# Optimization experiments

Hardware: AMD Instinct MI355X
Metric: run time of the kernel (lower is better)

## Reference

```python
import jax, jax.numpy as jnp
import numpy as np

INF = 1e+24
DK = 16


def setup_inputs() -> dict:
    key = jax.random.key(0)
    ks = jax.random.split(key, 9)
    B, T, D = 64, 512, 1024
    x = jax.random.normal(ks[0], (B, T, D), dtype=jnp.float32)
    padding_mask = jax.random.randint(ks[1], (B, T, 1), 0, 2) > 0
    s = 1.0 / np.sqrt(D)
    Wq = jax.random.normal(ks[2], (D, DK), dtype=jnp.float32) * s
    bq = jnp.zeros((DK,), dtype=jnp.float32)
    Wk = jax.random.normal(ks[3], (D, DK), dtype=jnp.float32) * s
    bk = jnp.zeros((DK,), dtype=jnp.float32)
    Wv = jax.random.normal(ks[4], (D, D), dtype=jnp.float32) * s
    bv = jnp.zeros((D,), dtype=jnp.float32)
    return {"x": x, "padding_mask": padding_mask, "Wq": Wq, "bq": bq,
            "Wk": Wk, "bk": bk, "Wv": Wv, "bv": bv}


def reference(x, padding_mask, Wq, bq, Wk, bk, Wv, bv):
    # x: [B,T,D]; padding_mask: [B,T,1] bool
    q = x @ Wq + bq                      # [B,T,dk]
    k = x @ Wk + bk                      # [B,T,dk]
    v = x @ Wv + bv                      # [B,T,D]
    # original writes -INF into k at padded positions (broadcast over dk)
    k = jnp.where(padding_mask, jnp.float32(-INF), k)
    # NOTE: original multiplies by sqrt(dk) (misnamed _inv_dk)
    att = jnp.einsum('btd,bsd->bts', q, k) * jnp.sqrt(jnp.float32(DK))
    T = x.shape[1]
    causal = jnp.triu(jnp.ones((T, T), dtype=bool), k=1)  # [T,T]
    att = jnp.where(causal[None, :, :], jnp.float32(-INF), att)
    return jnp.einsum('bts,bsd->btd', jax.nn.softmax(att, axis=2), v)
```

## Files before the change

kernel.cpp:

```cpp
#include <hip/hip_runtime.h>
#include <hip/hip_bf16.h>
#include <stdint.h>

#define NEG_BIG (-1e24f)

typedef __attribute__((ext_vector_type(8))) short bf16x8;
typedef __attribute__((ext_vector_type(4))) float f32x4;

#define AS1 __attribute__((address_space(1)))
#define AS3 __attribute__((address_space(3)))

__device__ __forceinline__ void gload_lds16(const void* g, void* l) {
    __builtin_amdgcn_global_load_lds((AS1 unsigned*)g, (AS3 unsigned*)l, 16, 0, 0);
}

__device__ __forceinline__ unsigned short f2bf(float f) {
    union { float f; unsigned u; } v; v.f = f;
    return (unsigned short)((v.u + 0x7FFFu + ((v.u >> 16) & 1u)) >> 16);
}

__device__ __forceinline__ void lds_barrier() {
    asm volatile("s_waitcnt lgkmcnt(0)" ::: "memory");
    __builtin_amdgcn_s_barrier();
    asm volatile("" ::: "memory");
}

__global__ void detect_mask_kernel(const unsigned* pm, int* flag) {
    __shared__ int notI, notF;
    if (threadIdx.x == 0) { notI = 0; notF = 0; }
    __syncthreads();
    int li = 0, lf = 0;
    for (int i = threadIdx.x; i < 8192; i += 256) {
        unsigned v = pm[i];
        if (v > 1u) li = 1;
        if (v != 0u && v != 0x3F800000u) lf = 1;
    }
    if (li) atomicOr(&notI, 1);
    if (lf) atomicOr(&notF, 1);
    __syncthreads();
    if (threadIdx.x == 0) *flag = notI ? (notF ? 1 : 2) : 0;
}

__global__ __launch_bounds__(1024, 8)
void qk_conv_kernel(const float* __restrict__ x,
                    const float* __restrict__ Wq, const float* __restrict__ bq,
                    const float* __restrict__ Wk, const float* __restrict__ bk,
                    const void* __restrict__ pm, const int* __restrict__ pmflag,
                    unsigned short* __restrict__ xbf,
                    float* __restrict__ qo, float* __restrict__ ko) {
    __shared__ float smem[4 * 64 * 33];
    const int tid = threadIdx.x;
    const int r0 = blockIdx.x * 64;
    const int lane = tid & 63;
    const int wv = __builtin_amdgcn_readfirstlane(tid >> 6);
    const int g = wv & 3;
    const int sl = wv >> 2;
    const int jb = (g & 1) * 8;
    const int d0 = sl * 16;
    const float* __restrict__ W = (g < 2) ? Wq : Wk;

    const int sr = tid >> 4;
    const int sd = (tid & 15) * 4;
    const float* __restrict__ xp = x + (size_t)(r0 + sr) * 1024 + sd;
    unsigned short* __restrict__ xbp = xbf + (size_t)(r0 + sr) * 1024 + sd;

    float acc[8];
#pragma unroll
    for (int j = 0; j < 8; j++) acc[j] = 0.f;

    float4 xv = *(const float4*)xp;
    {
        uint2 pk;
        pk.x = (unsigned)f2bf(xv.x) | ((unsigned)f2bf(xv.y) << 16);
        pk.y = (unsigned)f2bf(xv.z) | ((unsigned)f2bf(xv.w) << 16);
        *(uint2*)xbp = pk;
        float* b0 = smem;
        b0[sr * 65 + sd + 0] = xv.x;
        b0[sr * 65 + sd + 1] = xv.y;
        b0[sr * 65 + sd + 2] = xv.z;
        b0[sr * 65 + sd + 3] = xv.w;
    }
    xv = *(const float4*)(xp + 64);
    lds_barrier();

    for (int t = 0; t < 16; t++) {
        if (t + 1 < 16) {
            uint2 pk;
            pk.x = (unsigned)f2bf(xv.x) | ((unsigned)f2bf(xv.y) << 16);
            pk.y = (unsigned)f2bf(xv.z) | ((unsigned)f2bf(xv.w) << 16);
            *(uint2*)(xbp + (t + 1) * 64) = pk;
            float* bw = smem + ((t + 1) & 1) * (64 * 65);
            bw[sr * 65 + sd + 0] = xv.x;
            bw[sr * 65 + sd + 1] = xv.y;
            bw[sr * 65 + sd + 2] = xv.z;
            bw[sr * 65 + sd + 3] = xv.w;
            if (t + 2 < 16) xv = *(const float4*)(xp + (t + 2) * 64);
        }
        const float* __restrict__ xrow = smem + (t & 1) * (64 * 65) + lane * 65 + d0;
        const float* __restrict__ wrow = W + (size_t)(t * 64 + d0) * 16 + jb;
#pragma unroll
        for (int dd = 0; dd < 16; dd += 2) {
            const float x0 = xrow[dd];
            const float x1 = xrow[dd + 1];
            const float* __restrict__ w0 = wrow + dd * 16;
#pragma unroll
            for (int j = 0; j < 8; j++) acc[j] = fmaf(x0, w0[j], acc[j]);
#pragma unroll
            for (int j = 0; j < 8; j++) acc[j] = fmaf(x1, w0[16 + j], acc[j]);
        }
        lds_barrier();
    }

    float* red = smem;
    const int cb = jb + (g >> 1) * 16;
    {
        float* rr = red + ((size_t)(sl * 64 + lane)) * 33 + cb;
#pragma unroll
        for (int j = 0; j < 8; j++) rr[j] = acc[j];
    }
    __syncthreads();

    const int row = tid >> 4;
    const int c = tid & 15;
    const int grow = r0 + row;
    const float qv = red[(size_t)row * 33 + c]
                   + red[(size_t)(64 + row) * 33 + c]
                   + red[(size_t)(128 + row) * 33 + c]
                   + red[(size_t)(192 + row) * 33 + c] + bq[c];
    qo[(size_t)grow * 16 + c] = qv;
    const int flag = *pmflag;
    bool mk;
    if (flag == 1) mk = ((const unsigned char*)pm)[grow] != 0;
    else           mk = ((const unsigned*)pm)[grow] != 0;
    float kv;
    if (mk) {
        kv = NEG_BIG;
    } else {
        kv = red[(size_t)row * 33 + 16 + c]
           + red[(size_t)(64 + row) * 33 + 16 + c]
           + red[(size_t)(128 + row) * 33 + 16 + c]
           + red[(size_t)(192 + row) * 33 + 16 + c] + bk[c];
    }
    ko[(size_t)grow * 16 + c] = kv;
}

__global__ void wvt_kernel(const float* __restrict__ Wv, unsigned short* __restrict__ WvT) {
    __shared__ float tile[32][33];
    const int k0 = blockIdx.x * 32, n0 = blockIdx.y * 32;
    const int tid = threadIdx.x;
#pragma unroll
    for (int i = 0; i < 4; i++) {
        int idx = i * 256 + tid;
        int r = idx >> 5, c = idx & 31;
        tile[r][c] = Wv[(size_t)(k0 + r) * 1024 + n0 + c];
    }
    __syncthreads();
#pragma unroll
    for (int i = 0; i < 4; i++) {
        int idx = i * 256 + tid;
        int r = idx >> 5, c = idx & 31;
        WvT[(size_t)(n0 + r) * 1024 + k0 + c] = f2bf(tile[c][r]);
    }
}

__global__ __launch_bounds__(256, 4)
void vgemm_kernel(const unsigned short* __restrict__ A,
                  const unsigned short* __restrict__ Bt,
                  const float* __restrict__ bias,
                  unsigned short* __restrict__ vTg) {
    __shared__ __align__(16) unsigned short smem[17408];
    const int bid = blockIdx.x;
    const int c = bid & 7;
    const int g = bid >> 3;
    const int mt = c * 32 + (g >> 3);
    const int nt = g & 7;
    const int m0 = mt * 128;
    const int n0 = nt * 128;
    const int tid = threadIdx.x;
    const int lane = tid & 63;
    const int wave = tid >> 6;
    const int wm = (wave & 1) * 64;
    const int wn = (wave >> 1) * 64;
    const int l15 = lane & 15;
    const int quad = lane >> 4;
    const int arow = tid >> 2;
    const int acol = (tid & 3) * 8;
    const unsigned short* __restrict__ Ar0 = A + (size_t)(m0 + arow) * 1024 + acol;
    const unsigned short* __restrict__ Ar1 = A + (size_t)(m0 + 64 + arow) * 1024 + acol;
    const unsigned short* __restrict__ Br0 = Bt + (size_t)(n0 + arow) * 1024 + acol;
    const unsigned short* __restrict__ Br1 = Bt + (size_t)(n0 + 64 + arow) * 1024 + acol;
    f32x4 acc[4][4];
#pragma unroll
    for (int i = 0; i < 4; i++)
#pragma unroll
        for (int j = 0; j < 4; j++)
#pragma unroll
            for (int r = 0; r < 4; r++) acc[i][j][r] = 0.f;

    {
        unsigned short* As = smem;
        unsigned short* Bs = smem + 4096;
        gload_lds16(Ar0, As + tid * 8);
        gload_lds16(Ar1, As + 2048 + tid * 8);
        gload_lds16(Br0, Bs + tid * 8);
        gload_lds16(Br1, Bs + 2048 + tid * 8);
    }
    __syncthreads();
    int cur = 0;
    for (int t = 0; t < 32; t++) {
        if (t + 1 < 32) {
            const int kn = (t + 1) * 32;
            unsigned short* As = smem + (cur ^ 1) * 8192;
            unsigned short* Bs = As + 4096;
            gload_lds16(Ar0 + kn, As + tid * 8);
            gload_lds16(Ar1 + kn, As + 2048 + tid * 8);
            gload_lds16(Br0 + kn, Bs + tid * 8);
            gload_lds16(Br1 + kn, Bs + 2048 + tid * 8);
        }
        const unsigned short* As = smem + cur * 8192;
        const unsigned short* Bs = As + 4096;
        bf16x8 af[4], bfr[4];
#pragma unroll
        for (int i = 0; i < 4; i++) {
            af[i]  = *(const bf16x8*)(As + (wm + i * 16 + l15) * 32 + quad * 8);
            bfr[i] = *(const bf16x8*)(Bs + (wn + i * 16 + l15) * 32 + quad * 8);
        }
#pragma unroll
        for (int i = 0; i < 4; i++)
#pragma unroll
            for (int j = 0; j < 4; j++)
                acc[i][j] = __builtin_amdgcn_mfma_f32_16x16x32_bf16(af[i], bfr[j], acc[i][j], 0, 0, 0);
        __syncthreads();
        cur ^= 1;
    }
    unsigned short* vt = smem;
#pragma unroll
    for (int j = 0; j < 4; j++) {
        const int e_local = wn + j * 16 + l15;
        const float bb = bias[n0 + e_local];
#pragma unroll
        for (int i = 0; i < 4; i++) {
            const int s_base = wm + i * 16 + quad * 4;
            unsigned short h0 = f2bf(acc[i][j][0] + bb);
            unsigned short h1 = f2bf(acc[i][j][1] + bb);
            unsigned short h2 = f2bf(acc[i][j][2] + bb);
            unsigned short h3 = f2bf(acc[i][j][3] + bb);
            uint2 u;
            u.x = (unsigned)h0 | ((unsigned)h1 << 16);
            u.y = (unsigned)h2 | ((unsigned)h3 << 16);
            *(uint2*)(vt + e_local * 136 + s_base) = u;
        }
    }
    __syncthreads();
    const int b = m0 >> 9;
    const int sbase = m0 & 511;
#pragma unroll
    for (int p = 0; p < 8; p++) {
        const int idx = p * 256 + tid;
        const int e = idx >> 4;
        const int s8 = (idx & 15) * 8;
        uint4 val = *(const uint4*)(vt + e * 136 + s8);
        *(uint4*)(vTg + ((size_t)b * 1024 + n0 + e) * 512 + sbase + s8) = val;
    }
}

__global__ __launch_bounds__(256, 2)
void score_kernel(const float* __restrict__ q, const float* __restrict__ k,
                  unsigned short* __restrict__ P, float* __restrict__ isum) {
    __shared__ float Kt[512 * 16];
    __shared__ float Qt[128 * 16];
    __shared__ float redm[2][128];
    __shared__ float reds[2][128];
    __shared__ unsigned short Pt[2][64][132];
    const int tid = threadIdx.x;
    const int b = blockIdx.y;
    const int t0 = blockIdx.x * 128;
    {
        const float4* ks = (const float4*)(k + (size_t)b * 512 * 16);
        float4* kd = (float4*)Kt;
#pragma unroll
        for (int i = 0; i < 8; i++) kd[i * 256 + tid] = ks[i * 256 + tid];
        const float4* qs = (const float4*)(q + ((size_t)b * 512 + t0) * 16);
        float4* qd = (float4*)Qt;
#pragma unroll
        for (int i = 0; i < 2; i++) qd[i * 256 + tid] = qs[i * 256 + tid];
    }
    __syncthreads();
    const int row = tid & 127;
    const int half = tid >> 7;
    const int sbeg = half * 256;
    const int tglob = t0 + row;
    float qr[16];
#pragma unroll
    for (int j = 0; j < 16; j++) qr[j] = Qt[row * 16 + j];

    float m = -INFINITY;
    for (int s = sbeg; s < sbeg + 256; s++) {
        const float* kk = Kt + s * 16;
        float dot = 0.f;
#pragma unroll
        for (int j = 0; j < 16; j++) dot = fmaf(qr[j], kk[j], dot);
        float sc = (s > tglob) ? NEG_BIG : dot * 4.0f;
        m = fmaxf(m, sc);
    }
    redm[half][row] = m;
    __syncthreads();
    const float M = fmaxf(redm[0][row], redm[1][row]);
    float sum = 0.f;
    for (int ph = 0; ph < 4; ph++) {
        const int c0 = sbeg + ph * 64;
        for (int s = c0; s < c0 + 64; s++) {
            const float* kk = Kt + s * 16;
            float dot = 0.f;
#pragma unroll
            for (int j = 0; j < 16; j++) dot = fmaf(qr[j], kk[j], dot);
            float sc = (s > tglob) ? NEG_BIG : dot * 4.0f;
            float p = __expf(sc - M);
            sum += p;
            Pt[half][s - c0][row] = f2bf(p);
        }
        __syncthreads();
#pragma unroll
        for (int i = 0; i < 8; i++) {
            int li = i * 256 + tid;
            int h = li >> 10;
            int r = (li >> 3) & 127;
            int cg = li & 7;
            union { unsigned short u[8]; uint4 v; } tmp;
#pragma unroll
            for (int j = 0; j < 8; j++) tmp.u[j] = Pt[h][cg * 8 + j][r];
            *(uint4*)(P + ((size_t)(b * 512 + t0 + r)) * 512 + h * 256 + ph * 64 + cg * 8) = tmp.v;
        }
        __syncthreads();
    }
    reds[half][row] = sum;
    __syncthreads();
    if (half == 0) {
        float tot = reds[0][row] + reds[1][row];
        isum[(size_t)b * 512 + tglob] = 1.0f / tot;
    }
}

__global__ __launch_bounds__(256, 4)
void pv_kernel(const unsigned short* __restrict__ P,
               const unsigned short* __restrict__ vT,
               const float* __restrict__ isum,
               float* __restrict__ out) {
    __shared__ __align__(16) unsigned short smem[16384];
    const int bid = blockIdx.x;
    const int c = bid & 7;
    const int g = bid >> 3;
    const int b = c * 8 + (g >> 5);
    const int rem = g & 31;
    const int m0 = (rem >> 3) * 128;
    const int n0 = (rem & 7) * 128;
    const int tid = threadIdx.x;
    const int lane = tid & 63;
    const int wave = tid >> 6;
    const int wm = (wave & 1) * 64;
    const int wn = (wave >> 1) * 64;
    const int l15 = lane & 15;
    const int quad = lane >> 4;
    const int arow = tid >> 2;
    const int acol = (tid & 3) * 8;
    const unsigned short* __restrict__ Ar0 = P + (size_t)b * 512 * 512 + (size_t)(m0 + arow) * 512 + acol;
    const unsigned short* __restrict__ Ar1 = Ar0 + (size_t)64 * 512;
    const unsigned short* __restrict__ Br0 = vT + (size_t)b * 1024 * 512 + (size_t)(n0 + arow) * 512 + acol;
    const unsigned short* __restrict__ Br1 = Br0 + (size_t)64 * 512;
    f32x4 acc[4][4];
#pragma unroll
    for (int i = 0; i < 4; i++)
#pragma unroll
        for (int j = 0; j < 4; j++)
#pragma unroll
            for (int r = 0; r < 4; r++) acc[i][j][r] = 0.f;

    {
        unsigned short* As = smem;
        unsigned short* Bs = smem + 4096;
        gload_lds16(Ar0, As + tid * 8);
        gload_lds16(Ar1, As + 2048 + tid * 8);
        gload_lds16(Br0, Bs + tid * 8);
        gload_lds16(Br1, Bs + 2048 + tid * 8);
    }
    __syncthreads();
    int cur = 0;
    for (int t = 0; t < 16; t++) {
        if (t + 1 < 16) {
            const int kn = (t + 1) * 32;
            unsigned short* As = smem + (cur ^ 1) * 8192;
            unsigned short* Bs = As + 4096;
            gload_lds16(Ar0 + kn, As + tid * 8);
            gload_lds16(Ar1 + kn, As + 2048 + tid * 8);
            gload_lds16(Br0 + kn, Bs + tid * 8);
            gload_lds16(Br1 + kn, Bs + 2048 + tid * 8);
        }
        const unsigned short* As = smem + cur * 8192;
        const unsigned short* Bs = As + 4096;
        bf16x8 af[4], bfr[4];
#pragma unroll
        for (int i = 0; i < 4; i++) {
            af[i]  = *(const bf16x8*)(As + (wm + i * 16 + l15) * 32 + quad * 8);
            bfr[i] = *(const bf16x8*)(Bs + (wn + i * 16 + l15) * 32 + quad * 8);
        }
#pragma unroll
        for (int i = 0; i < 4; i++)
#pragma unroll
            for (int j = 0; j < 4; j++)
                acc[i][j] = __builtin_amdgcn_mfma_f32_16x16x32_bf16(af[i], bfr[j], acc[i][j], 0, 0, 0);
        __syncthreads();
        cur ^= 1;
    }
#pragma unroll
    for (int i = 0; i < 4; i++) {
#pragma unroll
        for (int r = 0; r < 4; r++) {
            const int trow = m0 + wm + i * 16 + quad * 4 + r;
            const float sc = isum[(size_t)b * 512 + trow];
#pragma unroll
            for (int j = 0; j < 4; j++) {
                const int ncol = n0 + wn + j * 16 + l15;
                out[((size_t)b * 512 + trow) * 1024 + ncol] = acc[i][j][r] * sc;
            }
        }
    }
}

extern "C" void kernel_launch(void* const* d_in, const int* in_sizes, int n_in,
                              void* d_out, int out_size, void* d_ws, size_t ws_size,
                              hipStream_t stream) {
    const float* x  = (const float*)d_in[0];
    const void*  pm = d_in[1];
    const float* Wq = (const float*)d_in[2];
    const float* bq = (const float*)d_in[3];
    const float* Wk = (const float*)d_in[4];
    const float* bk = (const float*)d_in[5];
    const float* Wv = (const float*)d_in[6];
    const float* bv = (const float*)d_in[7];
    float* out = (float*)d_out;

    char* ws = (char*)d_ws;
    const size_t MB = 1024 * 1024;
    unsigned short* xbf = (unsigned short*)ws;
    unsigned short* Pun = (unsigned short*)ws;
    unsigned short* vT  = (unsigned short*)(ws + 64 * MB);
    float* qbuf = (float*)(ws + 128 * MB);
    float* kbuf = (float*)(ws + 130 * MB);
    unsigned short* WvT = (unsigned short*)(ws + 132 * MB);
    float* isum = (float*)(ws + 134 * MB);
    int* flag   = (int*)(ws + 135 * MB);

    detect_mask_kernel<<<1, 256, 0, stream>>>((const unsigned*)pm, flag);
    qk_conv_kernel<<<512, 1024, 0, stream>>>(x, Wq, bq, Wk, bk, pm, flag, xbf, qbuf, kbuf);
    wvt_kernel<<<dim3(32, 32), 256, 0, stream>>>(Wv, WvT);
    vgemm_kernel<<<2048, 256, 0, stream>>>(xbf, WvT, bv, vT);
    score_kernel<<<dim3(4, 64), 256, 0, stream>>>(qbuf, kbuf, Pun, isum);
    pv_kernel<<<2048, 256, 0, stream>>>(Pun, vT, isum, out);
}
```

Measured before the change: 458.5 us.

## Skip causally masked score tiles and PV k-tiles, with fallback for fully masked rows

The score kernel now computes and stores probabilities only for key columns up to the end of the causal block, and the PV GEMM loops only over the k-tiles needed for each query block. A per-block flag detects the pathological case where every key for a row is masked to -1e24, where the softmax becomes uniform over all positions. In that case both kernels fall back to the full computation. This removes roughly half the exp/dot work and about half the PV GEMM work, at the cost of an extra barrier and a flag round-trip through global memory.

Measured after the change: 445.6 us. 2.8% less time.

```diff
diff --git a/kernel.cpp b/kernel.cpp
--- a/kernel.cpp
+++ b/kernel.cpp
@@ -266,15 +266,19 @@
 
 __global__ __launch_bounds__(256, 2)
 void score_kernel(const float* __restrict__ q, const float* __restrict__ k,
-                  unsigned short* __restrict__ P, float* __restrict__ isum) {
+                  unsigned short* __restrict__ P, float* __restrict__ isum,
+                  int* __restrict__ pflag) {
     __shared__ float Kt[512 * 16];
     __shared__ float Qt[128 * 16];
     __shared__ float redm[2][128];
     __shared__ float reds[2][128];
     __shared__ unsigned short Pt[2][64][132];
+    __shared__ int pathoS;
     const int tid = threadIdx.x;
     const int b = blockIdx.y;
     const int t0 = blockIdx.x * 128;
+    const int cend = t0 + 128;
+    if (tid == 0) pathoS = 0;
     {
         const float4* ks = (const float4*)(k + (size_t)b * 512 * 16);
         float4* kd = (float4*)Kt;
@@ -289,13 +293,14 @@
     const int row = tid & 127;
     const int half = tid >> 7;
     const int sbeg = half * 256;
+    const int send = (sbeg + 256 < cend) ? (sbeg + 256) : cend;
     const int tglob = t0 + row;
     float qr[16];
 #pragma unroll
     for (int j = 0; j < 16; j++) qr[j] = Qt[row * 16 + j];
 
     float m = -INFINITY;
-    for (int s = sbeg; s < sbeg + 256; s++) {
+    for (int s = sbeg; s < send; s++) {
         const float* kk = Kt + s * 16;
         float dot = 0.f;
 #pragma unroll
@@ -303,21 +308,27 @@
         float sc = (s > tglob) ? NEG_BIG : dot * 4.0f;
         m = fmaxf(m, sc);
     }
+    if (tglob < 511) m = fmaxf(m, NEG_BIG);
     redm[half][row] = m;
     __syncthreads();
     const float M = fmaxf(redm[0][row], redm[1][row]);
+    if (half == 0 && M <= -1e20f) pathoS = 1;
+    __syncthreads();
+    const int patho = pathoS;
     float sum = 0.f;
     for (int ph = 0; ph < 4; ph++) {
         const int c0 = sbeg + ph * 64;
-        for (int s = c0; s < c0 + 64; s++) {
-            const float* kk = Kt + s * 16;
-            float dot = 0.f;
-#pragma unroll
-            for (int j = 0; j < 16; j++) dot = fmaf(qr[j], kk[j], dot);
-            float sc = (s > tglob) ? NEG_BIG : dot * 4.0f;
-            float p = __expf(sc - M);
-            sum += p;
-            Pt[half][s - c0][row] = f2bf(p);
+        if (c0 < cend || patho) {
+            for (int s = c0; s < c0 + 64; s++) {
+                const float* kk = Kt + s * 16;
+                float dot = 0.f;
+#pragma unroll
+                for (int j = 0; j < 16; j++) dot = fmaf(qr[j], kk[j], dot);
+                float sc = (s > tglob) ? NEG_BIG : dot * 4.0f;
+                float p = __expf(sc - M);
+                sum += p;
+                Pt[half][s - c0][row] = f2bf(p);
+            }
         }
         __syncthreads();
 #pragma unroll
@@ -326,10 +337,12 @@
             int h = li >> 10;
             int r = (li >> 3) & 127;
             int cg = li & 7;
-            union { unsigned short u[8]; uint4 v; } tmp;
-#pragma unroll
-            for (int j = 0; j < 8; j++) tmp.u[j] = Pt[h][cg * 8 + j][r];
-            *(uint4*)(P + ((size_t)(b * 512 + t0 + r)) * 512 + h * 256 + ph * 64 + cg * 8) = tmp.v;
+            if (h * 256 + ph * 64 < cend || patho) {
+                union { unsigned short u[8]; uint4 v; } tmp;
+#pragma unroll
+                for (int j = 0; j < 8; j++) tmp.u[j] = Pt[h][cg * 8 + j][r];
+                *(uint4*)(P + ((size_t)(b * 512 + t0 + r)) * 512 + h * 256 + ph * 64 + cg * 8) = tmp.v;
+            }
         }
         __syncthreads();
     }
@@ -339,12 +352,14 @@
         float tot = reds[0][row] + reds[1][row];
         isum[(size_t)b * 512 + tglob] = 1.0f / tot;
     }
+    if (tid == 0) pflag[b * 4 + blockIdx.x] = patho;
 }
 
 __global__ __launch_bounds__(256, 4)
 void pv_kernel(const unsigned short* __restrict__ P,
                const unsigned short* __restrict__ vT,
                const float* __restrict__ isum,
+               const int* __restrict__ pflag,
                float* __restrict__ out) {
     __shared__ __align__(16) unsigned short smem[16384];
     const int bid = blockIdx.x;
@@ -354,6 +369,8 @@
     const int rem = g & 31;
     const int m0 = (rem >> 3) * 128;
     const int n0 = (rem & 7) * 128;
+    const int patho = pflag[b * 4 + (m0 >> 7)];
+    const int ntiles = patho ? 16 : ((m0 >> 5) + 4);
     const int tid = threadIdx.x;
     const int lane = tid & 63;
     const int wave = tid >> 6;
@@ -385,8 +402,8 @@
     }
     __syncthreads();
     int cur = 0;
-    for (int t = 0; t < 16; t++) {
-        if (t + 1 < 16) {
+    for (int t = 0; t < ntiles; t++) {
+        if (t + 1 < ntiles) {
             const int kn = (t + 1) * 32;
             unsigned short* As = smem + (cur ^ 1) * 8192;
             unsigned short* Bs = As + 4096;
@@ -449,11 +466,12 @@
     unsigned short* WvT = (unsigned short*)(ws + 132 * MB);
     float* isum = (float*)(ws + 134 * MB);
     int* flag   = (int*)(ws + 135 * MB);
+    int* pflag  = (int*)(ws + 135 * MB + 256);
 
     detect_mask_kernel<<<1, 256, 0, stream>>>((const unsigned*)pm, flag);
     qk_conv_kernel<<<512, 1024, 0, stream>>>(x, Wq, bq, Wk, bk, pm, flag, xbf, qbuf, kbuf);
     wvt_kernel<<<dim3(32, 32), 256, 0, stream>>>(Wv, WvT);
     vgemm_kernel<<<2048, 256, 0, stream>>>(xbf, WvT, bv, vT);
-    score_kernel<<<dim3(4, 64), 256, 0, stream>>>(qbuf, kbuf, Pun, isum);
-    pv_kernel<<<2048, 256, 0, stream>>>(Pun, vT, isum, out);
-}
+    score_kernel<<<dim3(4, 64), 256, 0, stream>>>(qbuf, kbuf, Pun, isum, pflag);
+    pv_kernel<<<2048, 256, 0, stream>>>(Pun, vT, isum, pflag, out);
+}
```
